# Optimization experiments

Hardware: AMD Instinct MI355X
Metric: run time of the kernel (lower is better)

## Reference

```python
import jax, jax.numpy as jnp
import numpy as np

D_MODEL = 512
EXPAND = 2
D_INNER = D_MODEL * EXPAND      # 1024
STATE = 64                      # N
DT_RANK = D_MODEL // 16         # 32
CONV_K = 4
K_WIN = 8                       # window of the approximate selective scan
LN_EPS = 1e-5


def setup_inputs() -> dict:
    key = jax.random.key(0)
    ks = jax.random.split(key, 8)
    norm = lambda k, shape, scale: (jax.random.normal(k, shape, jnp.float32) * scale)
    return {
        "x": jax.random.normal(ks[0], (1, 1024, D_MODEL), jnp.float32),
        "in_proj_w": norm(ks[1], (2 * D_INNER, D_MODEL), D_MODEL ** -0.5),
        "conv_w": norm(ks[2], (D_INNER, 1, CONV_K), 0.5),            # depthwise [O, I/g=1, K]
        "conv_b": jnp.zeros((D_INNER,), jnp.float32),
        "x_proj_w": norm(ks[3], (DT_RANK + 2 * STATE, D_INNER), D_INNER ** -0.5),
        "dt_proj_w": norm(ks[4], (D_INNER, DT_RANK), DT_RANK ** -0.5),
        "dt_proj_b": jnp.zeros((D_INNER,), jnp.float32),
        "A_log": jnp.broadcast_to(
            jnp.log(jnp.arange(1, STATE + 1, dtype=jnp.float32)), (D_INNER, STATE)
        ) + 0.0,
        "D_param": jnp.ones((D_INNER,), jnp.float32),
        "out_proj_w": norm(ks[5], (D_MODEL, D_INNER), D_INNER ** -0.5),
        "ln_w": jnp.ones((D_MODEL,), jnp.float32),
        "ln_b": jnp.zeros((D_MODEL,), jnp.float32),
    }


def _selective_scan(x, dt, A, Bp, Cp, Dp):
    """Windowed selective scan (faithful to the torch loop, vectorized).

    h_t = sum_{s=max(0,t-K+1)}^{t} exp(sum_{j=s+1}^{t} dt_j * A) * dt_s * B_s * x_s
    y_t = <h_t, C_t> + D * x_t
    x, dt: [B, L, d]; A: [d, N]; Bp, Cp: [B, L, N]; Dp: [d]
    """
    L = x.shape[1]
    K = min(L, K_WIN)
    log_dA = dt[..., None] * A                                # [B,L,d,N], <= 0
    dBx = dt[..., None] * Bp[:, :, None, :] * x[..., None]    # [B,L,d,N]
    cs = jnp.cumsum(log_dA, axis=1)                           # prefix sums of log-decay
    h = dBx
    for k in range(1, K):  # fixed small window, 7 iterations
        decay = jnp.exp(cs[:, k:] - cs[:, :-k])               # prod dA over (t-k, t]
        h = h.at[:, k:].add(decay * dBx[:, :-k])
    y = jnp.einsum('bldn,bln->bld', h, Cp) + Dp * x
    return y


def reference(x, in_proj_w, conv_w, conv_b, x_proj_w, dt_proj_w, dt_proj_b,
              A_log, D_param, out_proj_w, ln_w, ln_b):
    residual = x
    xz = x @ in_proj_w.T                                      # [B,L,2*d_inner]
    x_in, z = jnp.split(xz, 2, axis=-1)

    # causal depthwise conv1d (torch pads 3 both sides then keeps first L)
    xc = jnp.transpose(x_in, (0, 2, 1))                       # [B,d,L]
    xc = jax.lax.conv_general_dilated(
        xc, conv_w, window_strides=(1,), padding=[(CONV_K - 1, 0)],
        dimension_numbers=('NCH', 'OIH', 'NCH'), feature_group_count=D_INNER,
    ) + conv_b[None, :, None]
    xc = jax.nn.silu(jnp.transpose(xc, (0, 2, 1)))            # [B,L,d]

    x_dbl = xc @ x_proj_w.T                                   # [B,L,dt_rank+2N]
    dt, Bp, Cp = jnp.split(x_dbl, [DT_RANK, DT_RANK + STATE], axis=-1)
    dt = jax.nn.softplus(dt @ dt_proj_w.T + dt_proj_b)        # [B,L,d]
    A = -jnp.exp(A_log)                                       # [d,N]

    y = _selective_scan(xc, dt, A, Bp, Cp, D_param)
    y = y * jax.nn.silu(z)
    out = y @ out_proj_w.T + residual

    mu = out.mean(-1, keepdims=True)
    var = ((out - mu) ** 2).mean(-1, keepdims=True)
    return (out - mu) * jax.lax.rsqrt(var + LN_EPS) * ln_w + ln_b
```

## Files before the change

### kernel.cpp

```cpp
#include <hip/hip_runtime.h>
#include <hip/hip_fp16.h>
#include <math.h>

#define LSEQ    1024
#define DMODEL  512
#define DINNER  1024
#define NSTATE  64
#define NFUSED  1152
#define CHUNKT  64
#define TROWS   71

#define MB (1024u * 1024u)
#define XZ_OFF      (0)
#define XC_OFF      (8u * MB)
#define XCBF_OFF    (12u * MB)
#define XBF_OFF     (14u * MB)
#define INWBF_OFF   (15u * MB)
#define OUTWBF_OFF  (17u * MB)
#define WF_OFF      (18u * MB)
#define FUSED_OFF   (20u * MB + 256u * 1024)
#define BCHI_OFF    (24u * MB + 768u * 1024)
#define YBF_OFF     (25u * MB)
#define OUTPRE_OFF  (27u * MB)

typedef __attribute__((ext_vector_type(8))) short bf16x8;
typedef __attribute__((ext_vector_type(4))) float f32x4;

__device__ inline unsigned short f2bf(float f) {
  unsigned int u = __float_as_uint(f);
  u += 0x7fff + ((u >> 16) & 1);
  return (unsigned short)(u >> 16);
}

__global__ __launch_bounds__(256) void prep_kernel(
    const float* __restrict__ x, const float* __restrict__ inw,
    const float* __restrict__ outw, const float* __restrict__ xpw,
    const float* __restrict__ dtw, unsigned short* __restrict__ x_bf,
    unsigned short* __restrict__ inw_bf, unsigned short* __restrict__ outw_bf,
    unsigned short* __restrict__ Wf) {
  const int blk = blockIdx.x;
  if (blk < 2048) {
    const int i = blk * 256 + threadIdx.x;
    const float* src;
    unsigned short* dst;
    int j;
    if (i < 131072) {
      src = x; dst = x_bf; j = i;
    } else if (i < 393216) {
      src = inw; dst = inw_bf; j = i - 131072;
    } else {
      src = outw; dst = outw_bf; j = i - 393216;
    }
    const float4 v = *(const float4*)&src[(size_t)j * 4];
    ushort4 o;
    o.x = f2bf(v.x); o.y = f2bf(v.y); o.z = f2bf(v.z); o.w = f2bf(v.w);
    *(ushort4*)&dst[(size_t)j * 4] = o;
  } else {
    const int r = blk - 2048;
    if (r < 128) {
      for (int i = threadIdx.x; i < 1024; i += 256)
        Wf[(size_t)r * 1024 + i] = f2bf(xpw[(size_t)(32 + r) * 1024 + i]);
    } else {
      const int d = r - 128;
      __shared__ float w[32];
      if (threadIdx.x < 32) w[threadIdx.x] = dtw[d * 32 + threadIdx.x];
      __syncthreads();
      for (int i = threadIdx.x; i < 1024; i += 256) {
        float s = 0.f;
#pragma unroll
        for (int q = 0; q < 32; ++q) s = fmaf(w[q], xpw[(size_t)q * 1024 + i], s);
        Wf[(size_t)r * 1024 + i] = f2bf(s);
      }
    }
  }
}

template <int BM, int BN, int WM, int WN, bool RESID, bool WBCH>
__global__ __launch_bounds__(256) void gemm_bf(
    const unsigned short* __restrict__ A, const unsigned short* __restrict__ B,
    float* __restrict__ C, const float* __restrict__ resid,
    unsigned short* __restrict__ bch, int M, int N, int K) {
  constexpr int BK = 64;
  constexpr int WTM = BM / WM;
  constexpr int WTN = BN / WN;
  constexpr int FM = WTM / 16;
  constexpr int FN = WTN / 16;
  constexpr int APASS = (BM * BK * 2) / 4096;
  constexpr int BPASS = (BN * BK * 2) / 4096;

  __shared__ unsigned short As[2][BM * BK];
  __shared__ unsigned short Bs[2][BN * BK];

  const int tid = threadIdx.x;
  const int lane = tid & 63;
  const int wave = tid >> 6;
  const int wr = (wave / WN) * WTM;
  const int wc = (wave % WN) * WTN;
  const int bm = blockIdx.y * BM;
  const int bn = blockIdx.x * BN;

  auto stage = [&](int buf, int kt) {
#pragma unroll
    for (int p = 0; p < APASS; ++p) {
      const int e = (tid + p * 256) * 16;
      const int row = e >> 7;
      const int koff = (e & 127) >> 1;
      const unsigned short* src = A + (size_t)(bm + row) * K + kt + koff;
      __builtin_amdgcn_global_load_lds(
          (const __attribute__((address_space(1))) unsigned int*)src,
          (__attribute__((address_space(3))) unsigned int*)(&As[buf][e >> 1]),
          16, 0, 0);
    }
#pragma unroll
    for (int p = 0; p < BPASS; ++p) {
      const int e = (tid + p * 256) * 16;
      const int row = e >> 7;
      const int koff = (e & 127) >> 1;
      const unsigned short* src = B + (size_t)(bn + row) * K + kt + koff;
      __builtin_amdgcn_global_load_lds(
          (const __attribute__((address_space(1))) unsigned int*)src,
          (__attribute__((address_space(3))) unsigned int*)(&Bs[buf][e >> 1]),
          16, 0, 0);
    }
  };

  f32x4 acc[FM][FN];
#pragma unroll
  for (int m = 0; m < FM; ++m)
#pragma unroll
    for (int n = 0; n < FN; ++n) acc[m][n] = (f32x4){0.f, 0.f, 0.f, 0.f};

  const int nt = K / BK;
  stage(0, 0);
  __syncthreads();
  int cur = 0;
  for (int t = 0; t < nt; ++t) {
    if (t + 1 < nt) stage(cur ^ 1, (t + 1) * BK);
#pragma unroll
    for (int kk = 0; kk < BK / 32; ++kk) {
      bf16x8 a[FM], b[FN];
#pragma unroll
      for (int m = 0; m < FM; ++m)
        a[m] = *(const bf16x8*)(&As[cur][(wr + m * 16 + (lane & 15)) * BK +
                                         kk * 32 + (lane >> 4) * 8]);
#pragma unroll
      for (int n = 0; n < FN; ++n)
        b[n] = *(const bf16x8*)(&Bs[cur][(wc + n * 16 + (lane & 15)) * BK +
                                         kk * 32 + (lane >> 4) * 8]);
#pragma unroll
      for (int m = 0; m < FM; ++m)
#pragma unroll
        for (int n = 0; n < FN; ++n)
          acc[m][n] = __builtin_amdgcn_mfma_f32_16x16x32_bf16(a[m], b[n],
                                                              acc[m][n], 0, 0, 0);
    }
    __syncthreads();
    cur ^= 1;
  }

#pragma unroll
  for (int m = 0; m < FM; ++m)
#pragma unroll
    for (int n = 0; n < FN; ++n) {
      const int col = bn + wc + n * 16 + (lane & 15);
#pragma unroll
      for (int r = 0; r < 4; ++r) {
        const int row = bm + wr + m * 16 + (lane >> 4) * 4 + r;
        float v = acc[m][n][r];
        if (RESID) v += resid[(size_t)row * N + col];
        C[(size_t)row * N + col] = v;
        if (WBCH) {
          if (col < 128) {
            const int j = col & 63, hi = col >> 6;
            bch[(size_t)row * 128 + j * 2 + hi] =
                __half_as_ushort(__float2half(v));
          }
        }
      }
    }
}

__global__ __launch_bounds__(256) void conv_silu_kernel(
    const float* __restrict__ xz, const float* __restrict__ w,
    const float* __restrict__ b, float* __restrict__ xc,
    unsigned short* __restrict__ xc_bf) {
  const int idx = blockIdx.x * 256 + threadIdx.x;
  const int t = idx >> 10;
  const int d = idx & 1023;
  float acc = b[d];
#pragma unroll
  for (int j = 0; j < 4; ++j) {
    const int ts = t - 3 + j;
    if (ts >= 0) acc = fmaf(xz[(size_t)ts * 2048 + d], w[d * 4 + j], acc);
  }
  const float s = acc / (1.f + __expf(-acc));
  xc[idx] = s;
  xc_bf[idx] = f2bf(s);
}

__global__ __launch_bounds__(512) void scan_kernel(
    const float* __restrict__ fused,
    const unsigned int* __restrict__ bchi,
    const float* __restrict__ xc,
    const float* __restrict__ xz,
    const float* __restrict__ A_log,
    const float* __restrict__ dtb,
    const float* __restrict__ Dp,
    unsigned short* __restrict__ y_bf) {
  __shared__ unsigned int bch[TROWS * 64];
  __shared__ float2 dtl[TROWS * 8];
  __shared__ unsigned int auxl[CHUNKT * 8];

  const int tid = threadIdx.x;
  const int lane = tid & 63;
  const int wave = tid >> 6;
  const int d0 = blockIdx.x * 8;
  const int t0 = blockIdx.y * CHUNKT;
  const int T = t0 - 7;

#pragma unroll
  for (int p = 0; p < 3; ++p) {
    const int idx = p * 512 + tid;
    if (idx < TROWS * 16) {
      const int r = idx >> 4;
      const int off = idx & 15;
      const int gt = T + r;
      int4 v = make_int4(0, 0, 0, 0);
      if (gt >= 0) v = *(const int4*)((const char*)bchi + (size_t)gt * 256 + off * 16);
      *(int4*)((char*)bch + (size_t)idx * 16) = v;
    }
  }

  if (tid < 2 * TROWS) {
    const int row = tid >> 1;
    const int dloc = (tid & 1) * 4;
    const int gt = T + row;
    if (gt >= 0) {
      const float4 f  = *(const float4*)&fused[(size_t)gt * NFUSED + 128 + d0 + dloc];
      const float4 xv = *(const float4*)&xc[(size_t)gt * DINNER + d0 + dloc];
      const float4 zv = *(const float4*)&xz[(size_t)gt * 2048 + DINNER + d0 + dloc];
      const float4 dp = *(const float4*)&Dp[d0 + dloc];
      const float4 db = *(const float4*)&dtb[d0 + dloc];
      const float fa[4] = {f.x, f.y, f.z, f.w};
      const float xa[4] = {xv.x, xv.y, xv.z, xv.w};
      const float za[4] = {zv.x, zv.y, zv.z, zv.w};
      const float pa[4] = {dp.x, dp.y, dp.z, dp.w};
      const float ba[4] = {db.x, db.y, db.z, db.w};
#pragma unroll
      for (int q = 0; q < 4; ++q) {
        const float dtp = fa[q] + ba[q];
        const float dt = (dtp > 20.f) ? dtp : log1pf(__expf(dtp));
        dtl[row * 8 + dloc + q] = make_float2(dt, dt * xa[q]);
        if (row >= 7) {
          const float dxc = pa[q] * xa[q];
          const float sz = za[q] / (1.f + __expf(-za[q]));
          auxl[(row - 7) * 8 + dloc + q] =
              (unsigned int)__half_as_ushort(__float2half(dxc)) |
              ((unsigned int)__half_as_ushort(__float2half(sz)) << 16);
        }
      }
    } else {
#pragma unroll
      for (int q = 0; q < 4; ++q) dtl[row * 8 + dloc + q] = make_float2(0.f, 0.f);
    }
  }
  __syncthreads();

  const int d = d0 + wave;
  const float An = -__expf(A_log[(size_t)d * NSTATE + lane]);

  float ER[8], dB[8];
#pragma unroll
  for (int j = 1; j <= 7; ++j) {
    const float2 pk = dtl[(7 - j) * 8 + wave];
    const unsigned int bc = bch[(7 - j) * 64 + lane];
    const float Bp = __half2float(__ushort_as_half((unsigned short)(bc & 0xffffu)));
    ER[8 - j] = __expf(An * pk.x);
    dB[8 - j] = pk.y * Bp;
  }
  ER[0] = 1.f; dB[0] = 0.f;

  for (int sb = 0; sb < CHUNKT; sb += 8) {
#pragma unroll
    for (int qu = 0; qu < 2; ++qu) {
      float cc[4];
#pragma unroll
      for (int h4 = 0; h4 < 4; ++h4) {
        const int u = qu * 4 + h4;
        const int r = sb + u + 7;
        const float2 pk = dtl[r * 8 + wave];
        const unsigned int bc = bch[r * 64 + lane];
        const float Bp = __half2float(__ushort_as_half((unsigned short)(bc & 0xffffu)));
        const float Cp = __half2float(__ushort_as_half((unsigned short)(bc >> 16)));
        const float E0 = __expf(An * pk.x);
        const float dBt = pk.y * Bp;

        float s1 = dB[(u - 7) & 7];
#pragma unroll
        for (int k = 6; k >= 1; --k) {
          const int sl = (u - k) & 7;
          s1 = fmaf(ER[sl], s1, dB[sl]);
        }
        const float h = fmaf(E0, s1, dBt);
        ER[u] = E0;
        dB[u] = dBt;
        cc[h4] = h * Cp;
      }
      float a0 = cc[0] + __shfl_xor(cc[0], 1, 64);
      float a1 = cc[1] + __shfl_xor(cc[1], 1, 64);
      float a2 = cc[2] + __shfl_xor(cc[2], 1, 64);
      float a3 = cc[3] + __shfl_xor(cc[3], 1, 64);
      float p0 = (lane & 1) ? a1 : a0;
      float p1 = (lane & 1) ? a3 : a2;
      p0 += __shfl_xor(p0, 2, 64);
      p1 += __shfl_xor(p1, 2, 64);
      float rr = (lane & 2) ? p1 : p0;
      rr += __shfl_xor(rr, 4, 64);
      rr += __shfl_xor(rr, 8, 64);
      rr += __shfl_xor(rr, 16, 64);
      rr += __shfl_xor(rr, 32, 64);
      if (lane < 4) {
        const int s = sb + qu * 4 + lane;
        const unsigned int av = auxl[s * 8 + wave];
        const float dxc = __half2float(__ushort_as_half((unsigned short)(av & 0xffffu)));
        const float sz  = __half2float(__ushort_as_half((unsigned short)(av >> 16)));
        y_bf[(size_t)(t0 + s) * DINNER + d] = f2bf((rr + dxc) * sz);
      }
    }
  }
}

__global__ __launch_bounds__(256) void ln_kernel(
    const float* __restrict__ src, const float* __restrict__ w,
    const float* __restrict__ b, float* __restrict__ out) {
  const int t = blockIdx.x;
  const int i0 = threadIdx.x;
  const int i1 = threadIdx.x + 256;
  const float v0 = src[(size_t)t * DMODEL + i0];
  const float v1 = src[(size_t)t * DMODEL + i1];
  float s = v0 + v1;
  float q = v0 * v0 + v1 * v1;
#pragma unroll
  for (int m = 32; m; m >>= 1) {
    s += __shfl_xor(s, m, 64);
    q += __shfl_xor(q, m, 64);
  }
  __shared__ float ss[4], sq[4];
  const int wv = threadIdx.x >> 6;
  if ((threadIdx.x & 63) == 0) { ss[wv] = s; sq[wv] = q; }
  __syncthreads();
  s = ss[0] + ss[1] + ss[2] + ss[3];
  q = sq[0] + sq[1] + sq[2] + sq[3];
  const float mu = s * (1.f / 512.f);
  const float var = q * (1.f / 512.f) - mu * mu;
  const float inv = rsqrtf(var + 1e-5f);
  out[(size_t)t * DMODEL + i0] = (v0 - mu) * inv * w[i0] + b[i0];
  out[(size_t)t * DMODEL + i1] = (v1 - mu) * inv * w[i1] + b[i1];
}

extern "C" void kernel_launch(void* const* d_in, const int* in_sizes, int n_in,
                              void* d_out, int out_size, void* d_ws,
                              size_t ws_size, hipStream_t stream) {
  const float* x         = (const float*)d_in[0];
  const float* in_w      = (const float*)d_in[1];
  const float* conv_w    = (const float*)d_in[2];
  const float* conv_b    = (const float*)d_in[3];
  const float* xproj_w   = (const float*)d_in[4];
  const float* dtproj_w  = (const float*)d_in[5];
  const float* dtproj_b  = (const float*)d_in[6];
  const float* A_log     = (const float*)d_in[7];
  const float* Dp        = (const float*)d_in[8];
  const float* outproj_w = (const float*)d_in[9];
  const float* ln_w      = (const float*)d_in[10];
  const float* ln_b      = (const float*)d_in[11];
  float* out = (float*)d_out;

  char* ws = (char*)d_ws;
  float*          xz      = (float*)(ws + XZ_OFF);
  float*          xc      = (float*)(ws + XC_OFF);
  unsigned short* xc_bf   = (unsigned short*)(ws + XCBF_OFF);
  unsigned short* x_bf    = (unsigned short*)(ws + XBF_OFF);
  unsigned short* inw_bf  = (unsigned short*)(ws + INWBF_OFF);
  unsigned short* outw_bf = (unsigned short*)(ws + OUTWBF_OFF);
  unsigned short* Wf      = (unsigned short*)(ws + WF_OFF);
  float*          fused   = (float*)(ws + FUSED_OFF);
  unsigned short* bchi    = (unsigned short*)(ws + BCHI_OFF);
  unsigned short* y_bf    = (unsigned short*)(ws + YBF_OFF);
  float*          outpre  = (float*)(ws + OUTPRE_OFF);

  prep_kernel<<<3200, 256, 0, stream>>>(x, in_w, outproj_w, xproj_w, dtproj_w,
                                        x_bf, inw_bf, outw_bf, Wf);
  gemm_bf<64, 32, 2, 2, false, false>
      <<<dim3(2048 / 32, 1024 / 64), 256, 0, stream>>>(
          x_bf, inw_bf, xz, nullptr, nullptr, 1024, 2048, 512);
  conv_silu_kernel<<<(LSEQ * DINNER) / 256, 256, 0, stream>>>(xz, conv_w,
                                                              conv_b, xc, xc_bf);
  gemm_bf<64, 32, 2, 2, false, true>
      <<<dim3(NFUSED / 32, 1024 / 64), 256, 0, stream>>>(
          xc_bf, Wf, fused, nullptr, bchi, 1024, NFUSED, 1024);
  scan_kernel<<<dim3(DINNER / 8, LSEQ / CHUNKT), 512, 0, stream>>>(
      fused, (const unsigned int*)bchi, xc, xz, A_log, dtproj_b, Dp, y_bf);
  gemm_bf<32, 32, 2, 2, true, false>
      <<<dim3(512 / 32, 1024 / 32), 256, 0, stream>>>(
          y_bf, outw_bf, outpre, x, nullptr, 1024, 512, 1024);
  ln_kernel<<<LSEQ, 256, 0, stream>>>(outpre, ln_w, ln_b, out);
}
```

Before: 105.2 us.

## Transpose scan shared-memory layout, pair timesteps, stage y tile, shrink GEMM tiles

Stores the B/C and dt values in shared memory time-major per state lane, so each lane loads two consecutive timesteps with one vector read. The scan now processes timesteps in pairs and reduces eight outputs per butterfly, and it uses exp2f with a prescaled A. Outputs go to a shared tile and are written as 16-byte vectors instead of scattered 2-byte stores. The first two GEMMs also switch to 32-row tiles to launch more blocks; this adds shared-memory padding and some extra work in the window start-up.

Result: slower. 111.7 us (+6.2%).

```diff
diff --git a/kernel.cpp b/kernel.cpp
--- a/kernel.cpp
+++ b/kernel.cpp
@@ -8,7 +8,7 @@
 #define NSTATE  64
 #define NFUSED  1152
 #define CHUNKT  64
-#define TROWS   71
+#define PROWS   72
 
 #define MB (1024u * 1024u)
 #define XZ_OFF      (0)
@@ -30,6 +30,9 @@
   unsigned int u = __float_as_uint(f);
   u += 0x7fff + ((u >> 16) & 1);
   return (unsigned short)(u >> 16);
+}
+__device__ inline float h2f(unsigned short h) {
+  return __half2float(__ushort_as_half(h));
 }
 
 __global__ __launch_bounds__(256) void prep_kernel(
@@ -207,31 +210,31 @@
     const float* __restrict__ dtb,
     const float* __restrict__ Dp,
     unsigned short* __restrict__ y_bf) {
-  __shared__ unsigned int bch[TROWS * 64];
-  __shared__ float2 dtl[TROWS * 8];
+  __shared__ unsigned int bch2[64 * 74];
+  __shared__ float2 dtl2[8 * PROWS];
   __shared__ unsigned int auxl[CHUNKT * 8];
+  __shared__ unsigned short ytile[CHUNKT * 8];
 
   const int tid = threadIdx.x;
   const int lane = tid & 63;
   const int wave = tid >> 6;
   const int d0 = blockIdx.x * 8;
   const int t0 = blockIdx.y * CHUNKT;
-  const int T = t0 - 7;
-
-#pragma unroll
-  for (int p = 0; p < 3; ++p) {
-    const int idx = p * 512 + tid;
-    if (idx < TROWS * 16) {
-      const int r = idx >> 4;
-      const int off = idx & 15;
-      const int gt = T + r;
-      int4 v = make_int4(0, 0, 0, 0);
-      if (gt >= 0) v = *(const int4*)((const char*)bchi + (size_t)gt * 256 + off * 16);
-      *(int4*)((char*)bch + (size_t)idx * 16) = v;
-    }
-  }
-
-  if (tid < 2 * TROWS) {
+  const int T = t0 - 8;
+
+  for (int i = tid; i < PROWS * 16; i += 512) {
+    const int p = i >> 4;
+    const int c4 = (i & 15) * 4;
+    const int gt = T + p;
+    uint4 v = make_uint4(0u, 0u, 0u, 0u);
+    if (gt >= 0) v = *(const uint4*)&bchi[(size_t)gt * 64 + c4];
+    bch2[(c4 + 0) * 74 + p] = v.x;
+    bch2[(c4 + 1) * 74 + p] = v.y;
+    bch2[(c4 + 2) * 74 + p] = v.z;
+    bch2[(c4 + 3) * 74 + p] = v.w;
+  }
+
+  if (tid < 2 * PROWS) {
     const int row = tid >> 1;
     const int dloc = (tid & 1) * 4;
     const int gt = T + row;
@@ -250,83 +253,100 @@
       for (int q = 0; q < 4; ++q) {
         const float dtp = fa[q] + ba[q];
         const float dt = (dtp > 20.f) ? dtp : log1pf(__expf(dtp));
-        dtl[row * 8 + dloc + q] = make_float2(dt, dt * xa[q]);
-        if (row >= 7) {
+        dtl2[(dloc + q) * PROWS + row] = make_float2(dt, dt * xa[q]);
+        if (row >= 8) {
           const float dxc = pa[q] * xa[q];
           const float sz = za[q] / (1.f + __expf(-za[q]));
-          auxl[(row - 7) * 8 + dloc + q] =
+          auxl[(row - 8) * 8 + dloc + q] =
               (unsigned int)__half_as_ushort(__float2half(dxc)) |
               ((unsigned int)__half_as_ushort(__float2half(sz)) << 16);
         }
       }
     } else {
 #pragma unroll
-      for (int q = 0; q < 4; ++q) dtl[row * 8 + dloc + q] = make_float2(0.f, 0.f);
+      for (int q = 0; q < 4; ++q)
+        dtl2[(dloc + q) * PROWS + row] = make_float2(0.f, 0.f);
     }
   }
   __syncthreads();
 
   const int d = d0 + wave;
-  const float An = -__expf(A_log[(size_t)d * NSTATE + lane]);
+  const float An2 = -__expf(A_log[(size_t)d * NSTATE + lane]) * 1.44269504f;
 
   float ER[8], dB[8];
 #pragma unroll
-  for (int j = 1; j <= 7; ++j) {
-    const float2 pk = dtl[(7 - j) * 8 + wave];
-    const unsigned int bc = bch[(7 - j) * 64 + lane];
-    const float Bp = __half2float(__ushort_as_half((unsigned short)(bc & 0xffffu)));
-    ER[8 - j] = __expf(An * pk.x);
-    dB[8 - j] = pk.y * Bp;
-  }
-  ER[0] = 1.f; dB[0] = 0.f;
+  for (int p = 0; p < 8; ++p) {
+    const float2 pk = dtl2[wave * PROWS + p];
+    const unsigned int bc = bch2[lane * 74 + p];
+    ER[p] = exp2f(An2 * pk.x);
+    dB[p] = pk.y * h2f((unsigned short)(bc & 0xffffu));
+  }
 
   for (int sb = 0; sb < CHUNKT; sb += 8) {
-#pragma unroll
-    for (int qu = 0; qu < 2; ++qu) {
-      float cc[4];
-#pragma unroll
-      for (int h4 = 0; h4 < 4; ++h4) {
-        const int u = qu * 4 + h4;
-        const int r = sb + u + 7;
-        const float2 pk = dtl[r * 8 + wave];
-        const unsigned int bc = bch[r * 64 + lane];
-        const float Bp = __half2float(__ushort_as_half((unsigned short)(bc & 0xffffu)));
-        const float Cp = __half2float(__ushort_as_half((unsigned short)(bc >> 16)));
-        const float E0 = __expf(An * pk.x);
-        const float dBt = pk.y * Bp;
-
-        float s1 = dB[(u - 7) & 7];
-#pragma unroll
-        for (int k = 6; k >= 1; --k) {
-          const int sl = (u - k) & 7;
-          s1 = fmaf(ER[sl], s1, dB[sl]);
-        }
-        const float h = fmaf(E0, s1, dBt);
-        ER[u] = E0;
-        dB[u] = dBt;
-        cc[h4] = h * Cp;
+    float cc[8];
+#pragma unroll
+    for (int up = 0; up < 4; ++up) {
+      const int u = up * 2;
+      const int p = sb + 8 + u;
+      const float4 pk2 = *(const float4*)&dtl2[wave * PROWS + p];
+      const uint2 bc2 = *(const uint2*)&bch2[lane * 74 + p];
+      const float B0 = h2f((unsigned short)(bc2.x & 0xffffu));
+      const float C0 = h2f((unsigned short)(bc2.x >> 16));
+      const float B1 = h2f((unsigned short)(bc2.y & 0xffffu));
+      const float C1 = h2f((unsigned short)(bc2.y >> 16));
+      const float E0 = exp2f(An2 * pk2.x);
+      const float E1 = exp2f(An2 * pk2.z);
+      const float dB0 = pk2.y * B0;
+      const float dB1 = pk2.w * B1;
+
+      float sx = dB[(u - 7) & 7];
+      float sy = dB[(u - 6) & 7];
+#pragma unroll
+      for (int k = 6; k >= 2; --k) {
+        sx = fmaf(ER[(u - k) & 7], sx, dB[(u - k) & 7]);
+        sy = fmaf(ER[(u + 1 - k) & 7], sy, dB[(u + 1 - k) & 7]);
       }
-      float a0 = cc[0] + __shfl_xor(cc[0], 1, 64);
-      float a1 = cc[1] + __shfl_xor(cc[1], 1, 64);
-      float a2 = cc[2] + __shfl_xor(cc[2], 1, 64);
-      float a3 = cc[3] + __shfl_xor(cc[3], 1, 64);
-      float p0 = (lane & 1) ? a1 : a0;
-      float p1 = (lane & 1) ? a3 : a2;
-      p0 += __shfl_xor(p0, 2, 64);
-      p1 += __shfl_xor(p1, 2, 64);
-      float rr = (lane & 2) ? p1 : p0;
-      rr += __shfl_xor(rr, 4, 64);
-      rr += __shfl_xor(rr, 8, 64);
-      rr += __shfl_xor(rr, 16, 64);
-      rr += __shfl_xor(rr, 32, 64);
-      if (lane < 4) {
-        const int s = sb + qu * 4 + lane;
-        const unsigned int av = auxl[s * 8 + wave];
-        const float dxc = __half2float(__ushort_as_half((unsigned short)(av & 0xffffu)));
-        const float sz  = __half2float(__ushort_as_half((unsigned short)(av >> 16)));
-        y_bf[(size_t)(t0 + s) * DINNER + d] = f2bf((rr + dxc) * sz);
-      }
-    }
+      sx = fmaf(ER[(u - 1) & 7], sx, dB[(u - 1) & 7]);
+      sy = fmaf(E0, sy, dB0);
+      const float h0 = fmaf(E0, sx, dB0);
+      const float h1 = fmaf(E1, sy, dB1);
+      ER[u] = E0;     dB[u] = dB0;
+      ER[u + 1] = E1; dB[u + 1] = dB1;
+      cc[u] = h0 * C0;
+      cc[u + 1] = h1 * C1;
+    }
+    float a[8];
+#pragma unroll
+    for (int i = 0; i < 8; ++i) a[i] = cc[i] + __shfl_xor(cc[i], 1, 64);
+    float b0 = (lane & 1) ? a[1] : a[0];
+    float b1 = (lane & 1) ? a[3] : a[2];
+    float b2 = (lane & 1) ? a[5] : a[4];
+    float b3 = (lane & 1) ? a[7] : a[6];
+    b0 += __shfl_xor(b0, 2, 64);
+    b1 += __shfl_xor(b1, 2, 64);
+    b2 += __shfl_xor(b2, 2, 64);
+    b3 += __shfl_xor(b3, 2, 64);
+    float c0 = (lane & 2) ? b1 : b0;
+    float c1 = (lane & 2) ? b3 : b2;
+    c0 += __shfl_xor(c0, 4, 64);
+    c1 += __shfl_xor(c1, 4, 64);
+    float r = (lane & 4) ? c1 : c0;
+    r += __shfl_xor(r, 8, 64);
+    r += __shfl_xor(r, 16, 64);
+    r += __shfl_xor(r, 32, 64);
+    if (lane < 8) {
+      const int s = sb + lane;
+      const unsigned int av = auxl[s * 8 + wave];
+      const float dxc = h2f((unsigned short)(av & 0xffffu));
+      const float sz  = h2f((unsigned short)(av >> 16));
+      ytile[s * 8 + wave] = f2bf((r + dxc) * sz);
+    }
+  }
+
+  __syncthreads();
+  if (tid < CHUNKT) {
+    const uint4 vy = *(const uint4*)&ytile[tid * 8];
+    *(uint4*)&y_bf[(size_t)(t0 + tid) * DINNER + d0] = vy;
   }
 }
 
@@ -390,13 +410,13 @@
 
   prep_kernel<<<3200, 256, 0, stream>>>(x, in_w, outproj_w, xproj_w, dtproj_w,
                                         x_bf, inw_bf, outw_bf, Wf);
-  gemm_bf<64, 32, 2, 2, false, false>
-      <<<dim3(2048 / 32, 1024 / 64), 256, 0, stream>>>(
+  gemm_bf<32, 32, 2, 2, false, false>
+      <<<dim3(2048 / 32, 1024 / 32), 256, 0, stream>>>(
           x_bf, inw_bf, xz, nullptr, nullptr, 1024, 2048, 512);
   conv_silu_kernel<<<(LSEQ * DINNER) / 256, 256, 0, stream>>>(xz, conv_w,
                                                               conv_b, xc, xc_bf);
-  gemm_bf<64, 32, 2, 2, false, true>
-      <<<dim3(NFUSED / 32, 1024 / 64), 256, 0, stream>>>(
+  gemm_bf<32, 32, 2, 2, false, true>
+      <<<dim3(NFUSED / 32, 1024 / 32), 256, 0, stream>>>(
           xc_bf, Wf, fused, nullptr, bchi, 1024, NFUSED, 1024);
   scan_kernel<<<dim3(DINNER / 8, LSEQ / CHUNKT), 512, 0, stream>>>(
       fused, (const unsigned int*)bchi, xc, xz, A_log, dtproj_b, Dp, y_bf);
```
